# Kernel tuning notes

Hardware: AMD Instinct MI355X
Metric: run time of the kernel (lower is better)

Reference implementation:

```python
import jax, jax.numpy as jnp
import numpy as np

H = 16          # n_heads
DH = 128        # head_dim
DR = 64         # rope_dim
DC = DH - DR    # content_dim = 64
THETA = 10000.0
SCALE = 1.0 / np.sqrt(DH)


def _rope_tables(T, dtype):
    inv = 1.0 / (THETA ** (jnp.arange(0, DR, 2, dtype=jnp.float32) / DR))  # [DR/2]
    t = jnp.arange(T, dtype=jnp.float32)
    freqs = jnp.outer(t, inv)  # [T, DR/2]
    return jnp.cos(freqs).astype(dtype), jnp.sin(freqs).astype(dtype)


def _apply_rope(x, cos, sin):
    # x: [B,H,T,DR]; cos/sin: [T,DR/2] broadcast over B,H
    d = x.shape[-1] // 2
    x1, x2 = x[..., :d], x[..., d:]
    return jnp.concatenate([x1 * cos - x2 * sin, x1 * sin + x2 * cos], axis=-1)


def setup_inputs() -> dict:
    key = jax.random.key(0)
    ks = jax.random.split(key, 9)
    B, T, D = 1, 2048, 2048
    s = 0.02
    return {
        "x": jax.random.normal(ks[0], (B, T, D), jnp.float32),
        "Wq_down": jax.random.normal(ks[1], (D, 512), jnp.float32) * s,
        "Wq_up": jax.random.normal(ks[2], (512, H * DC), jnp.float32) * s,
        "Wq_rope": jax.random.normal(ks[3], (D, H * DR), jnp.float32) * s,
        "Wkv_down": jax.random.normal(ks[4], (D, 512), jnp.float32) * s,
        "Wk_up": jax.random.normal(ks[5], (512, H * DC), jnp.float32) * s,
        "Wv_up": jax.random.normal(ks[6], (512, H * DH), jnp.float32) * s,
        "Wk_rope": jax.random.normal(ks[7], (D, H * DR), jnp.float32) * s,
        "Wo": jax.random.normal(ks[8], (H * DH, D), jnp.float32) * s,
    }


def reference(x, Wq_down, Wq_up, Wq_rope, Wkv_down, Wk_up, Wv_up, Wk_rope, Wo):
    B, T, D = x.shape
    # low-rank query path: down then up, content part only
    q_content = ((x @ Wq_down) @ Wq_up).reshape(B, T, H, DC).transpose(0, 2, 1, 3)
    q_pos = (x @ Wq_rope).reshape(B, T, H, DR).transpose(0, 2, 1, 3)
    kv_latent = x @ Wkv_down                    # [B,T,d_latent]
    k_pos = (x @ Wk_rope).reshape(B, T, H, DR).transpose(0, 2, 1, 3)

    cos, sin = _rope_tables(T, x.dtype)
    q_pos = _apply_rope(q_pos, cos, sin)
    k_pos = _apply_rope(k_pos, cos, sin)

    k_content = (kv_latent @ Wk_up).reshape(B, T, H, DC).transpose(0, 2, 1, 3)
    v = (kv_latent @ Wv_up).reshape(B, T, H, DH).transpose(0, 2, 1, 3)

    q = jnp.concatenate([q_content, q_pos], axis=-1)  # [B,H,T,DH]
    k = jnp.concatenate([k_content, k_pos], axis=-1)  # [B,H,T,DH]

    scores = jnp.einsum("bhtd,bhsd->bhts", q, k) * SCALE
    causal = jnp.tril(jnp.ones((T, T), dtype=bool))
    scores = jnp.where(causal, scores, jnp.finfo(scores.dtype).min)
    attn = jax.nn.softmax(scores, axis=-1)
    out = jnp.einsum("bhts,bhsd->bhtd", attn, v)       # [B,H,T,DH]
    out = out.transpose(0, 2, 1, 3).reshape(B, T, H * DH)
    return out @ Wo
```

## Files before the change

### kernel.cpp

```cpp
#include <hip/hip_runtime.h>
#include <math.h>

#define T_SEQ 2048
#define D_MODEL 2048
#define H_HEADS 16
#define DH 128
#define DR 64
#define DC 64
#define D_LAT 512
#define NSPLIT 3
#define QSCALE (0.08838834764831845f * 1.4426950408889634f)

typedef __attribute__((ext_vector_type(8))) short short8;
typedef __attribute__((ext_vector_type(4))) short short4v;
typedef __attribute__((ext_vector_type(4))) float f32x4;

__device__ __forceinline__ float bf2f(short b) {
    unsigned u = ((unsigned)(unsigned short)b) << 16;
    return __builtin_bit_cast(float, u);
}
__device__ __forceinline__ short f2bf(float f) {
    unsigned u = __builtin_bit_cast(unsigned, f);
    unsigned r = u + 0x7fffu + ((u >> 16) & 1u);
    return (short)(r >> 16);
}
__device__ __forceinline__ short f2bf_trunc(float f) {
    return (short)(__builtin_bit_cast(unsigned, f) >> 16);
}

#define GLD_LDS(gp, lp) \
    __builtin_amdgcn_global_load_lds( \
        (const __attribute__((address_space(1))) void*)(gp), \
        (__attribute__((address_space(3))) void*)(lp), 16, 0, 0)

__device__ __forceinline__ void ct_tile(float (*tile)[33],
                                        const float* __restrict__ W,
                                        short* __restrict__ Wt,
                                        int R, int C, int ldo, int rel) {
    int bx = rel % (C / 32), by = rel / (C / 32);
    int c0 = bx * 32, r0 = by * 32;
    int tx = threadIdx.x & 31, ty = threadIdx.x >> 5;
    #pragma unroll
    for (int i = 0; i < 4; ++i)
        tile[ty + i * 8][tx] = W[(size_t)(r0 + ty + i * 8) * C + c0 + tx];
    __syncthreads();
    #pragma unroll
    for (int i = 0; i < 4; ++i)
        Wt[(size_t)(c0 + ty + i * 8) * ldo + r0 + tx] = f2bf(tile[tx][ty + i * 8]);
    __syncthreads();
}

__global__ __launch_bounds__(256) void prep(const float* __restrict__ x,
                                            short* __restrict__ xb,
                                            const float* __restrict__ Wqd,
                                            const float* __restrict__ Wkvd,
                                            const float* __restrict__ Wqr,
                                            const float* __restrict__ Wkr,
                                            const float* __restrict__ Wqu,
                                            const float* __restrict__ Wku,
                                            const float* __restrict__ Wvu,
                                            const float* __restrict__ Wo,
                                            short* __restrict__ WdT,
                                            short* __restrict__ WupT2,
                                            short* __restrict__ WoT) {
    __shared__ float tile[32][33];
    int bid = blockIdx.x;
    if (bid < 4096) {
        int i = bid * 1024 + threadIdx.x * 4;
        float4 f = *(const float4*)&x[i];
        short4v o;
        o.x = f2bf(f.x); o.y = f2bf(f.y); o.z = f2bf(f.z); o.w = f2bf(f.w);
        *(short4v*)&xb[i] = o;
    } else if (bid < 5120) {
        ct_tile(tile, Wqd,  WdT + (size_t)0 * 2048,    2048, 512,  2048, bid - 4096);
    } else if (bid < 6144) {
        ct_tile(tile, Wkvd, WdT + (size_t)512 * 2048,  2048, 512,  2048, bid - 5120);
    } else if (bid < 8192) {
        ct_tile(tile, Wqr,  WdT + (size_t)1024 * 2048, 2048, 1024, 2048, bid - 6144);
    } else if (bid < 10240) {
        ct_tile(tile, Wkr,  WdT + (size_t)2048 * 2048, 2048, 1024, 2048, bid - 8192);
    } else if (bid < 10752) {
        ct_tile(tile, Wqu,  WupT2 + (size_t)0 * 512,    512, 1024, 512, bid - 10240);
    } else if (bid < 11264) {
        ct_tile(tile, Wku,  WupT2 + (size_t)1024 * 512, 512, 1024, 512, bid - 10752);
    } else if (bid < 12288) {
        ct_tile(tile, Wvu,  WupT2 + (size_t)2048 * 512, 512, 2048, 512, bid - 11264);
    } else {
        ct_tile(tile, Wo,   WoT, 2048, 2048, 2048, bid - 12288);
    }
}

__global__ __launch_bounds__(256) void transpose_bf16(const short* __restrict__ in,
                                                      short* __restrict__ outb,
                                                      int ldi) {
    __shared__ short tile[64][65];
    int c0 = blockIdx.x * 64, t0 = blockIdx.y * 64;
    int tx = threadIdx.x & 31, ty = threadIdx.x >> 5;
    #pragma unroll
    for (int i = 0; i < 8; ++i) {
        int r = ty + i * 8;
        int vv = *(const int*)&in[(size_t)(t0 + r) * ldi + c0 + tx * 2];
        tile[r][tx * 2]     = (short)(vv & 0xffff);
        tile[r][tx * 2 + 1] = (short)(((unsigned)vv) >> 16);
    }
    __syncthreads();
    #pragma unroll
    for (int i = 0; i < 8; ++i) {
        int c = ty + i * 8;
        unsigned lo = (unsigned short)tile[tx * 2][c];
        unsigned hi = (unsigned short)tile[tx * 2 + 1][c];
        *(int*)&outb[(size_t)(c0 + c) * 2048 + t0 + tx * 2] = (int)(lo | (hi << 16));
    }
}

__global__ __launch_bounds__(256) void gemm_bt(const short* __restrict__ A,
                                               const short* __restrict__ A2,
                                               const short* __restrict__ Bt,
                                               short* __restrict__ C0,
                                               short* __restrict__ C1,
                                               short* __restrict__ C2,
                                               short* __restrict__ C3,
                                               int N, int Kblk,
                                               int lda, int ldb, int ldc,
                                               int ncut, int scut, float cscale) {
    __shared__ short As[128 * 32];
    __shared__ short Bs[128 * 32];
    const int tid = threadIdx.x;
    const int wave = tid >> 6, lane = tid & 63;
    const int lin = blockIdx.x;
    const int X = N >> 7, Xq = X >> 2;
    const int xcd = lin & 7;
    int r = lin >> 3;
    const int bx = (xcd & 3) * Xq + (r % Xq); r /= Xq;
    const int by = (xcd >> 2) * 8 + (r & 7);
    const int bz = r >> 3;
    const int row0 = by * 128, col0 = bx * 128;
    const int kbase = bz * Kblk;
    const short* Ause = (col0 < ncut) ? A : A2;
    short* Cuse = (bz == 0) ? C0 : (bz == 1) ? C1 : (bz == 2) ? C2 : C3;
    const int wr = (wave >> 1) * 64, wc = (wave & 1) * 64;
    const int lr = lane & 15, quad = lane >> 4;

    f32x4 acc[4][4];
    #pragma unroll
    for (int i = 0; i < 4; ++i)
        #pragma unroll
        for (int j = 0; j < 4; ++j) acc[i][j] = (f32x4){0.f, 0.f, 0.f, 0.f};

    for (int k0 = kbase; k0 < kbase + Kblk; k0 += 32) {
        __syncthreads();
        #pragma unroll
        for (int it = 0; it < 2; ++it) {
            int idx = wave * 64 + it * 256 + lane;
            const short* ga = Ause + (size_t)(row0 + (idx >> 2)) * lda + k0 + (idx & 3) * 8;
            const short* gb = Bt   + (size_t)(col0 + (idx >> 2)) * ldb + k0 + (idx & 3) * 8;
            int lds0 = (wave * 64 + it * 256) * 8;
            GLD_LDS(ga, &As[lds0]);
            GLD_LDS(gb, &Bs[lds0]);
        }
        __syncthreads();

        short8 af[4], bfr[4];
        #pragma unroll
        for (int i = 0; i < 4; ++i)
            af[i] = *(const short8*)&As[(wr + i * 16 + lr) * 32 + quad * 8];
        #pragma unroll
        for (int j = 0; j < 4; ++j)
            bfr[j] = *(const short8*)&Bs[(wc + j * 16 + lr) * 32 + quad * 8];
        #pragma unroll
        for (int i = 0; i < 4; ++i)
            #pragma unroll
            for (int j = 0; j < 4; ++j)
                acc[i][j] = __builtin_amdgcn_mfma_f32_16x16x32_bf16(af[i], bfr[j],
                                                                   acc[i][j], 0, 0, 0);
    }

    const float sc = (col0 < scut) ? cscale : 1.0f;
    #pragma unroll
    for (int i = 0; i < 4; ++i) {
        int rb = row0 + wr + i * 16 + quad * 4;
        #pragma unroll
        for (int j = 0; j < 4; ++j) {
            int c = col0 + wc + j * 16 + lr;
            #pragma unroll
            for (int rr = 0; rr < 4; ++rr)
                Cuse[(size_t)(rb + rr) * ldc + c] = f2bf(acc[i][j][rr] * sc);
        }
    }
}

__global__ __launch_bounds__(256) void add_bf16(short* __restrict__ a,
                                                const short* __restrict__ b) {
    int i = (blockIdx.x * 256 + threadIdx.x) * 8;
    short8 av = *(const short8*)&a[i];
    short8 bv = *(const short8*)&b[i];
    short8 o;
    #pragma unroll
    for (int j = 0; j < 8; ++j) o[j] = f2bf(bf2f(av[j]) + bf2f(bv[j]));
    *(short8*)&a[i] = o;
}

__global__ __launch_bounds__(256) void add_out_f32(const short* __restrict__ p0,
                                                   const short* __restrict__ p1,
                                                   const short* __restrict__ p2,
                                                   const short* __restrict__ p3,
                                                   float* __restrict__ out) {
    int i = (blockIdx.x * 256 + threadIdx.x) * 4;
    short4v a = *(const short4v*)&p0[i];
    short4v b = *(const short4v*)&p1[i];
    short4v c = *(const short4v*)&p2[i];
    short4v d = *(const short4v*)&p3[i];
    float4 o;
    o.x = (bf2f(a.x) + bf2f(b.x)) + (bf2f(c.x) + bf2f(d.x));
    o.y = (bf2f(a.y) + bf2f(b.y)) + (bf2f(c.y) + bf2f(d.y));
    o.z = (bf2f(a.z) + bf2f(b.z)) + (bf2f(c.z) + bf2f(d.z));
    o.w = (bf2f(a.w) + bf2f(b.w)) + (bf2f(c.w) + bf2f(d.w));
    *(float4*)&out[i] = o;
}

__global__ __launch_bounds__(256) void rope_cat(short* __restrict__ cat) {
    int idx = blockIdx.x * 256 + threadIdx.x;
    int i = idx & 31;
    int h = (idx >> 5) & (H_HEADS - 1);
    int t = (idx >> 9) & (T_SEQ - 1);
    int which = idx >> 20;
    size_t base = (size_t)t * 3072 + 1024 + which * 1024 + h * DR;
    float x1 = bf2f(cat[base + i]);
    float x2 = bf2f(cat[base + 32 + i]);
    float freq = (float)t * __powf(10000.0f, -(float)i / 32.0f);
    float c = cosf(freq), s = sinf(freq);
    float sc = which ? 1.0f : QSCALE;
    cat[base + i]      = f2bf((x1 * c - x2 * s) * sc);
    cat[base + 32 + i] = f2bf((x1 * s + x2 * c) * sc);
}

__global__ __launch_bounds__(256) void attn_mla_split(const short* __restrict__ qkup,
                                                      const short* __restrict__ cat,
                                                      const short* __restrict__ vT,
                                                      short* __restrict__ Opart01,
                                                      short* __restrict__ Opart2,
                                                      float* __restrict__ lpart) {
    const int lin = blockIdx.x;
    const int xcd = lin & 7;
    int r_ = lin >> 3;
    const int h = xcd + 8 * (r_ & 1);
    r_ >>= 1;
    const int qt = 31 - (r_ & 31);
    const int g = r_ >> 5;
    const int tid = threadIdx.x;
    const int wave = tid >> 6, lane = tid & 63;
    const int lr = lane & 15, quad = lane >> 4;

    __shared__ short Ks[32 * 128];
    __shared__ short Vst[128 * 32];
    __shared__ short Ps[4][16 * 40];

    short* Og = (g < 2) ? Opart01 + (size_t)g * (T_SEQ * 2048) : Opart2;
    const short8 ones = {0x3F80, 0x3F80, 0x3F80, 0x3F80,
                         0x3F80, 0x3F80, 0x3F80, 0x3F80};

    const int Q0 = qt * 64;
    const int qrow0 = Q0 + wave * 16;
    const int nchunk = 2 * qt + 2;
    const int qmax = qrow0 + 15;

    short8 qf[4];
    {
        int t = qrow0 + lr;
        #pragma unroll
        for (int kci = 0; kci < 4; ++kci) {
            const short* src = (kci < 2)
                ? qkup + (size_t)t * 4096 + h * 64
                : cat + (size_t)t * 3072 + 1024 + h * 64;
            qf[kci] = *(const short8*)&src[(kci & 1) * 32 + quad * 8];
        }
    }

    f32x4 Oacc[8];
    #pragma unroll
    for (int d = 0; d < 8; ++d) Oacc[d] = (f32x4){0.f, 0.f, 0.f, 0.f};
    f32x4 Lacc = (f32x4){0.f, 0.f, 0.f, 0.f};

    for (int c = g; c < nchunk; c += NSPLIT) {
        const int s0 = c * 32;
        __syncthreads();
        #pragma unroll
        for (int it = 0; it < 2; ++it) {
            int idx = wave * 64 + it * 256 + lane;
            int lds0 = (wave * 64 + it * 256) * 8;
            int key = idx >> 4, ch = idx & 15;
            int cg = ch ^ (key & 15);
            const short* gk = (cg < 8)
                ? qkup + (size_t)(s0 + key) * 4096 + 1024 + h * 64 + cg * 8
                : cat + (size_t)(s0 + key) * 3072 + 2048 + h * 64 + (cg - 8) * 8;
            GLD_LDS(gk, &Ks[lds0]);
            int d = idx >> 2, cp = idx & 3;
            int scg = cp ^ (d & 3);
            const short* gv = vT + (size_t)(h * 128 + d) * 2048 + s0 + scg * 8;
            GLD_LDS(gv, &Vst[lds0]);
        }
        __syncthreads();
        if (s0 > qmax) continue;

        f32x4 sacc[2];
        #pragma unroll
        for (int n = 0; n < 2; ++n) {
            sacc[n] = (f32x4){0.f, 0.f, 0.f, 0.f};
            #pragma unroll
            for (int kci = 0; kci < 4; ++kci) {
                short8 kf = *(const short8*)
                    &Ks[(n * 16 + lr) * 128 + ((kci * 4 + quad) ^ lr) * 8];
                sacc[n] = __builtin_amdgcn_mfma_f32_16x16x32_bf16(qf[kci], kf,
                                                                 sacc[n], 0, 0, 0);
            }
        }
        if (s0 + 31 > qrow0) {
            #pragma unroll
            for (int r = 0; r < 4; ++r) {
                int qg = qrow0 + quad * 4 + r;
                #pragma unroll
                for (int n = 0; n < 2; ++n) {
                    int s = s0 + n * 16 + lr;
                    sacc[n][r] = (s <= qg) ? sacc[n][r] : -1e30f;
                }
            }
        }
        #pragma unroll
        for (int r = 0; r < 4; ++r) {
            Ps[wave][(quad * 4 + r) * 40 + lr]      = f2bf_trunc(exp2f(sacc[0][r]));
            Ps[wave][(quad * 4 + r) * 40 + 16 + lr] = f2bf_trunc(exp2f(sacc[1][r]));
        }
        short8 pf = *(const short8*)&Ps[wave][lr * 40 + quad * 8];
        Lacc = __builtin_amdgcn_mfma_f32_16x16x32_bf16(pf, ones, Lacc, 0, 0, 0);
        #pragma unroll
        for (int dt = 0; dt < 8; ++dt) {
            short8 vf = *(const short8*)
                &Vst[(dt * 16 + lr) * 32 + (quad ^ (lr & 3)) * 8];
            Oacc[dt] = __builtin_amdgcn_mfma_f32_16x16x32_bf16(pf, vf,
                                                              Oacc[dt], 0, 0, 0);
        }
    }

    #pragma unroll
    for (int r = 0; r < 4; ++r) {
        int t = qrow0 + quad * 4 + r;
        #pragma unroll
        for (int dt = 0; dt < 8; ++dt)
            Og[(size_t)t * 2048 + h * 128 + dt * 16 + lr] = f2bf(Oacc[dt][r]);
    }
    if (lr == 0) {
        #pragma unroll
        for (int r = 0; r < 4; ++r) {
            int t = qrow0 + quad * 4 + r;
            lpart[(size_t)(g * T_SEQ + t) * H_HEADS + h] = Lacc[r];
        }
    }
}

__global__ __launch_bounds__(256) void attn_combine(const short* __restrict__ O01,
                                                    const short* __restrict__ O2,
                                                    const float* __restrict__ lpart,
                                                    short* __restrict__ ao) {
    const int t = blockIdx.x;
    const int h = blockIdx.y * 2 + (threadIdx.x >> 7);
    const int d = threadIdx.x & 127;
    size_t off = (size_t)t * 2048 + h * 128 + d;
    float num = bf2f(O01[off]) + bf2f(O01[(size_t)T_SEQ * 2048 + off]) + bf2f(O2[off]);
    float den = lpart[(size_t)(0 * T_SEQ + t) * H_HEADS + h] +
                lpart[(size_t)(1 * T_SEQ + t) * H_HEADS + h] +
                lpart[(size_t)(2 * T_SEQ + t) * H_HEADS + h];
    ao[off] = f2bf(num / den);
}

extern "C" void kernel_launch(void* const* d_in, const int* in_sizes, int n_in,
                              void* d_out, int out_size, void* d_ws, size_t ws_size,
                              hipStream_t stream) {
    const float* x        = (const float*)d_in[0];
    const float* Wq_down  = (const float*)d_in[1];
    const float* Wq_up    = (const float*)d_in[2];
    const float* Wq_rope  = (const float*)d_in[3];
    const float* Wkv_down = (const float*)d_in[4];
    const float* Wk_up    = (const float*)d_in[5];
    const float* Wv_up    = (const float*)d_in[6];
    const float* Wk_rope  = (const float*)d_in[7];
    const float* Wo       = (const float*)d_in[8];
    float* out = (float*)d_out;

    short* p = (short*)d_ws;
    short* xb     = p; p += (size_t)2048 * 2048;
    short* WoT    = p; p += (size_t)2048 * 2048;
    short* cat    = p; p += (size_t)2048 * 3072;
    short* upcat2 = p; p += (size_t)2048 * 4096;
    short* WdT    = p; p += (size_t)3072 * 2048;
    short* WupT2  = p; p += (size_t)4096 * 512;
    short* vT     = p; p += (size_t)2048 * 2048;
    float* lpart  = (float*)p;
    short* pdown   = upcat2;
    short* aob     = cat;
    short* Opart01 = WdT;
    short* Opart2  = xb;
    short* pw0     = upcat2;
    short* pw1     = upcat2 + (size_t)2048 * 2048;
    short* pw2     = WdT;
    short* pw3     = WdT + (size_t)2048 * 2048;

    prep<<<dim3(16384), 256, 0, stream>>>(x, xb, Wq_down, Wkv_down, Wq_rope,
                                          Wk_rope, Wq_up, Wk_up, Wv_up, Wo,
                                          WdT, WupT2, WoT);

    gemm_bt<<<dim3(24 * 16 * 2), 256, 0, stream>>>(xb, xb, WdT, cat, pdown,
                                                   nullptr, nullptr,
                                                   3072, 1024,
                                                   2048, 2048, 3072, 1 << 30, 0, 1.f);
    add_bf16<<<dim3(2048 * 3072 / 2048), 256, 0, stream>>>(cat, pdown);

    rope_cat<<<dim3(2 * T_SEQ * H_HEADS * 32 / 256), 256, 0, stream>>>(cat);

    gemm_bt<<<dim3(32 * 16 * 1), 256, 0, stream>>>(cat, cat + 512, WupT2,
                                                   upcat2, nullptr, nullptr, nullptr,
                                                   4096, 512,
                                                   3072, 512, 4096, 1024, 1024, QSCALE);

    transpose_bf16<<<dim3(32, 32), 256, 0, stream>>>(upcat2 + 2048, vT, 4096);

    attn_mla_split<<<dim3(32 * 16 * NSPLIT), 256, 0, stream>>>(upcat2, cat, vT,
                                                               Opart01, Opart2, lpart);
    attn_combine<<<dim3(2048, 8), 256, 0, stream>>>(Opart01, Opart2, lpart, aob);

    gemm_bt<<<dim3(16 * 16 * 4), 256, 0, stream>>>(aob, aob, WoT, pw0, pw1, pw2, pw3,
                                                   2048, 512,
                                                   2048, 2048, 2048, 1 << 30, 0, 1.f);
    add_out_f32<<<dim3(2048 * 2048 / 1024), 256, 0, stream>>>(pw0, pw1, pw2, pw3, out);
}
```

Before: 294.9 us.

## Fuse split-K add with RoPE, vectorize combine, hoist attention load addresses

Merges the split-K partial add and the RoPE/scale pass into one finish_down kernel, so the down-projection output is read and written once instead of twice. Vectorizes attn_combine to 8 bf16 elements per thread and replaces the per-element divide with one reciprocal per row. In the attention kernel, K/V global-to-LDS addresses are precomputed once and advanced by pointer increments instead of being recomputed every chunk, and exp2f is swapped for the hardware exp2 builtin. Together these cut launch count and integer and memory overhead, at a small risk to exp accuracy.

Result: faster. 285.9 us (-3.0%).

```diff
diff --git a/kernel.cpp b/kernel.cpp
--- a/kernel.cpp
+++ b/kernel.cpp
@@ -14,6 +14,12 @@
 typedef __attribute__((ext_vector_type(8))) short short8;
 typedef __attribute__((ext_vector_type(4))) short short4v;
 typedef __attribute__((ext_vector_type(4))) float f32x4;
+
+#if __has_builtin(__builtin_amdgcn_exp2f)
+#define EXP2(x) __builtin_amdgcn_exp2f(x)
+#else
+#define EXP2(x) exp2f(x)
+#endif
 
 __device__ __forceinline__ float bf2f(short b) {
     unsigned u = ((unsigned)(unsigned short)b) << 16;
@@ -189,15 +195,40 @@
     }
 }
 
-__global__ __launch_bounds__(256) void add_bf16(short* __restrict__ a,
-                                                const short* __restrict__ b) {
-    int i = (blockIdx.x * 256 + threadIdx.x) * 8;
-    short8 av = *(const short8*)&a[i];
-    short8 bv = *(const short8*)&b[i];
-    short8 o;
-    #pragma unroll
-    for (int j = 0; j < 8; ++j) o[j] = f2bf(bf2f(av[j]) + bf2f(bv[j]));
-    *(short8*)&a[i] = o;
+__global__ __launch_bounds__(192) void finish_down(short* __restrict__ cat,
+                                                   const short* __restrict__ pdown) {
+    const int t = blockIdx.x;
+    const int k8 = threadIdx.x * 8;
+    const int c0 = ((k8 >> 5) << 6) + (k8 & 31);
+    const size_t lo = (size_t)t * 3072 + c0;
+    const size_t hi = lo + 32;
+    short8 al = *(const short8*)&cat[lo];
+    short8 ah = *(const short8*)&cat[hi];
+    short8 bl = *(const short8*)&pdown[lo];
+    short8 bh = *(const short8*)&pdown[hi];
+    float xl[8], xh[8];
+    #pragma unroll
+    for (int j = 0; j < 8; ++j) {
+        xl[j] = bf2f(al[j]) + bf2f(bl[j]);
+        xh[j] = bf2f(ah[j]) + bf2f(bh[j]);
+    }
+    if (c0 >= 1024) {
+        float sc = (c0 < 2048) ? QSCALE : 1.0f;
+        #pragma unroll
+        for (int j = 0; j < 8; ++j) {
+            int i = (c0 & 31) + j;
+            float freq = (float)t * __powf(10000.0f, -(float)i / 32.0f);
+            float cs = cosf(freq), sn = sinf(freq);
+            float r1 = (xl[j] * cs - xh[j] * sn) * sc;
+            float r2 = (xl[j] * sn + xh[j] * cs) * sc;
+            xl[j] = r1; xh[j] = r2;
+        }
+    }
+    short8 ol, oh;
+    #pragma unroll
+    for (int j = 0; j < 8; ++j) { ol[j] = f2bf(xl[j]); oh[j] = f2bf(xh[j]); }
+    *(short8*)&cat[lo] = ol;
+    *(short8*)&cat[hi] = oh;
 }
 
 __global__ __launch_bounds__(256) void add_out_f32(const short* __restrict__ p0,
@@ -218,22 +249,6 @@
     *(float4*)&out[i] = o;
 }
 
-__global__ __launch_bounds__(256) void rope_cat(short* __restrict__ cat) {
-    int idx = blockIdx.x * 256 + threadIdx.x;
-    int i = idx & 31;
-    int h = (idx >> 5) & (H_HEADS - 1);
-    int t = (idx >> 9) & (T_SEQ - 1);
-    int which = idx >> 20;
-    size_t base = (size_t)t * 3072 + 1024 + which * 1024 + h * DR;
-    float x1 = bf2f(cat[base + i]);
-    float x2 = bf2f(cat[base + 32 + i]);
-    float freq = (float)t * __powf(10000.0f, -(float)i / 32.0f);
-    float c = cosf(freq), s = sinf(freq);
-    float sc = which ? 1.0f : QSCALE;
-    cat[base + i]      = f2bf((x1 * c - x2 * s) * sc);
-    cat[base + 32 + i] = f2bf((x1 * s + x2 * c) * sc);
-}
-
 __global__ __launch_bounds__(256) void attn_mla_split(const short* __restrict__ qkup,
                                                       const short* __restrict__ cat,
                                                       const short* __restrict__ vT,
@@ -276,6 +291,25 @@
         }
     }
 
+    const int idx = wave * 64 + lane;
+    const int key = idx >> 4;
+    const int cg = (idx & 15) ^ (key & 15);
+    const short* kp0 = (cg < 8)
+        ? qkup + (size_t)key * 4096 + 1024 + h * 64 + cg * 8
+        : cat + (size_t)key * 3072 + 2048 + h * 64 + (cg - 8) * 8;
+    const int kst = (cg < 8) ? 4096 : 3072;
+    const short* kp1 = kp0 + (size_t)16 * kst;
+    const int dd = idx >> 2;
+    const int scg = (idx & 3) ^ (dd & 3);
+    const short* vp0 = vT + (size_t)(h * 128 + dd) * 2048 + scg * 8;
+    const short* vp1 = vp0 + (size_t)64 * 2048;
+    kp0 += (size_t)g * 32 * kst; kp1 += (size_t)g * 32 * kst;
+    vp0 += g * 32;               vp1 += g * 32;
+    const int kadv = NSPLIT * 32 * kst;
+    const int vadv = NSPLIT * 32;
+    const int ldsA = (wave * 64) * 8;
+    const int ldsB = (wave * 64 + 256) * 8;
+
     f32x4 Oacc[8];
     #pragma unroll
     for (int d = 0; d < 8; ++d) Oacc[d] = (f32x4){0.f, 0.f, 0.f, 0.f};
@@ -284,21 +318,11 @@
     for (int c = g; c < nchunk; c += NSPLIT) {
         const int s0 = c * 32;
         __syncthreads();
-        #pragma unroll
-        for (int it = 0; it < 2; ++it) {
-            int idx = wave * 64 + it * 256 + lane;
-            int lds0 = (wave * 64 + it * 256) * 8;
-            int key = idx >> 4, ch = idx & 15;
-            int cg = ch ^ (key & 15);
-            const short* gk = (cg < 8)
-                ? qkup + (size_t)(s0 + key) * 4096 + 1024 + h * 64 + cg * 8
-                : cat + (size_t)(s0 + key) * 3072 + 2048 + h * 64 + (cg - 8) * 8;
-            GLD_LDS(gk, &Ks[lds0]);
-            int d = idx >> 2, cp = idx & 3;
-            int scg = cp ^ (d & 3);
-            const short* gv = vT + (size_t)(h * 128 + d) * 2048 + s0 + scg * 8;
-            GLD_LDS(gv, &Vst[lds0]);
-        }
+        GLD_LDS(kp0, &Ks[ldsA]);
+        GLD_LDS(kp1, &Ks[ldsB]);
+        GLD_LDS(vp0, &Vst[ldsA]);
+        GLD_LDS(vp1, &Vst[ldsB]);
+        kp0 += kadv; kp1 += kadv; vp0 += vadv; vp1 += vadv;
         __syncthreads();
         if (s0 > qmax) continue;
 
@@ -327,8 +351,8 @@
         }
         #pragma unroll
         for (int r = 0; r < 4; ++r) {
-            Ps[wave][(quad * 4 + r) * 40 + lr]      = f2bf_trunc(exp2f(sacc[0][r]));
-            Ps[wave][(quad * 4 + r) * 40 + 16 + lr] = f2bf_trunc(exp2f(sacc[1][r]));
+            Ps[wave][(quad * 4 + r) * 40 + lr]      = f2bf_trunc(EXP2(sacc[0][r]));
+            Ps[wave][(quad * 4 + r) * 40 + 16 + lr] = f2bf_trunc(EXP2(sacc[1][r]));
         }
         short8 pf = *(const short8*)&Ps[wave][lr * 40 + quad * 8];
         Lacc = __builtin_amdgcn_mfma_f32_16x16x32_bf16(pf, ones, Lacc, 0, 0, 0);
@@ -362,14 +386,21 @@
                                                     const float* __restrict__ lpart,
                                                     short* __restrict__ ao) {
     const int t = blockIdx.x;
-    const int h = blockIdx.y * 2 + (threadIdx.x >> 7);
-    const int d = threadIdx.x & 127;
-    size_t off = (size_t)t * 2048 + h * 128 + d;
-    float num = bf2f(O01[off]) + bf2f(O01[(size_t)T_SEQ * 2048 + off]) + bf2f(O2[off]);
+    const int h = threadIdx.x >> 4;
+    const int di = (threadIdx.x & 15) * 8;
+    size_t off = (size_t)t * 2048 + h * 128 + di;
+    short8 a = *(const short8*)&O01[off];
+    short8 b = *(const short8*)&O01[(size_t)T_SEQ * 2048 + off];
+    short8 c = *(const short8*)&O2[off];
     float den = lpart[(size_t)(0 * T_SEQ + t) * H_HEADS + h] +
                 lpart[(size_t)(1 * T_SEQ + t) * H_HEADS + h] +
                 lpart[(size_t)(2 * T_SEQ + t) * H_HEADS + h];
-    ao[off] = f2bf(num / den);
+    float inv = 1.0f / den;
+    short8 o;
+    #pragma unroll
+    for (int j = 0; j < 8; ++j)
+        o[j] = f2bf((bf2f(a[j]) + bf2f(b[j]) + bf2f(c[j])) * inv);
+    *(short8*)&ao[off] = o;
 }
 
 extern "C" void kernel_launch(void* const* d_in, const int* in_sizes, int n_in,
@@ -412,9 +443,8 @@
                                                    nullptr, nullptr,
                                                    3072, 1024,
                                                    2048, 2048, 3072, 1 << 30, 0, 1.f);
-    add_bf16<<<dim3(2048 * 3072 / 2048), 256, 0, stream>>>(cat, pdown);
-
-    rope_cat<<<dim3(2 * T_SEQ * H_HEADS * 32 / 256), 256, 0, stream>>>(cat);
+
+    finish_down<<<dim3(2048), 192, 0, stream>>>(cat, pdown);
 
     gemm_bt<<<dim3(32 * 16 * 1), 256, 0, stream>>>(cat, cat + 512, WupT2,
                                                    upcat2, nullptr, nullptr, nullptr,
@@ -425,7 +455,7 @@
 
     attn_mla_split<<<dim3(32 * 16 * NSPLIT), 256, 0, stream>>>(upcat2, cat, vT,
                                                                Opart01, Opart2, lpart);
-    attn_combine<<<dim3(2048, 8), 256, 0, stream>>>(Opart01, Opart2, lpart, aob);
+    attn_combine<<<dim3(2048), 256, 0, stream>>>(Opart01, Opart2, lpart, aob);
 
     gemm_bt<<<dim3(16 * 16 * 4), 256, 0, stream>>>(aob, aob, WoT, pw0, pw1, pw2, pw3,
                                                    2048, 512,
```
